# Kernel tuning notes

Hardware: AMD Instinct MI355X
Metric: run time of the kernel (lower is better)

Reference implementation:

```python
import jax, jax.numpy as jnp
import numpy as np

N = 50000      # num_nodes
R = 16         # num_relations
D = 200        # hidden_dim
E = 400000     # num_edges


def rgcn_layer(x, W, root, b, src, dst, etype):
    # Per-relation transform of all nodes: [R, N, D]
    xw = jnp.einsum('nd,rde->rne', x, W)
    # Per-edge message: gather transformed source feature for the edge's relation
    msg = xw[etype, src]                      # [E, D]
    # Mean aggregation per (relation, destination) pair, matching PyG RGCNConv aggr='mean'
    seg = etype * N + dst                     # composite segment id in [0, R*N)
    sums = jax.ops.segment_sum(msg, seg, num_segments=R * N)          # [R*N, D]
    cnt = jax.ops.segment_sum(jnp.ones((msg.shape[0],), x.dtype), seg,
                              num_segments=R * N)                     # [R*N]
    mean = sums / jnp.clip(cnt, 1.0)[:, None]
    agg = mean.reshape(R, N, -1).sum(0)       # sum over relations: [N, D]
    return agg + x @ root + b


def setup_inputs() -> dict:
    key = jax.random.key(0)
    ks = jax.random.split(key, 9)
    scale = 1.0 / np.sqrt(D)
    inp = {
        'edge_index': jax.random.randint(ks[0], (2, E), 0, N),
        'edge_type': jax.random.randint(ks[1], (E,), 0, R),
        'emb': jax.random.normal(ks[2], (N, D), jnp.float32),
        'W1': jax.random.normal(ks[3], (R, D, D), jnp.float32) * scale,
        'root1': jax.random.normal(ks[4], (D, D), jnp.float32) * scale,
        'b1': jnp.zeros((D,), jnp.float32),
        'W2': jax.random.normal(ks[5], (R, D, D), jnp.float32) * scale,
        'root2': jax.random.normal(ks[6], (D, D), jnp.float32) * scale,
        'b2': jnp.zeros((D,), jnp.float32),
    }
    return inp


def reference(edge_index, edge_type, emb, W1, root1, b1, W2, root2, b2):
    src, dst = edge_index[0], edge_index[1]
    h = rgcn_layer(emb, W1, root1, b1, src, dst, edge_type)
    h = jax.nn.relu(h)
    out = rgcn_layer(h, W2, root2, b2, src, dst, edge_type)
    return out
```

## Files before the change

### kernel.cpp

```cpp
#include <hip/hip_runtime.h>
#include <cstdint>
#include <cstddef>

#define NNODES 50000
#define NREL   16
#define DIM    200
#define NEDGE  400000
#define NBLK   782
#define NKEY   (NBLK * 1024)
#define NPART  (NKEY / 256)
#define WTREL  46592
#define WTSZ   (17 * WTREL)
#define MAXB   12
#define PCAP   1280
#define GTOT   119
#define BFRAG  13312

typedef __attribute__((ext_vector_type(8))) short short8;
typedef __attribute__((ext_vector_type(4))) float floatx4;

typedef __attribute__((address_space(1))) const unsigned int gas_u32;
typedef __attribute__((address_space(3))) unsigned int las_u32;

__device__ __forceinline__ unsigned short f2bf(float f) {
    unsigned int u = __float_as_uint(f);
    u = (u + 0x7FFFu + ((u >> 16) & 1u)) >> 16;
    return (unsigned short)u;
}
__device__ __forceinline__ float bf2f(unsigned short h) {
    return __uint_as_float(((unsigned int)h) << 16);
}


__device__ __forceinline__ int edge_key(int d, int r) {
    return (d >> 6) * 1024 + r * 64 + (d & 63);
}

__global__ void count_kernel(const int* __restrict__ ei, const int* __restrict__ et,
                             int* __restrict__ cnt) {
    int e = blockIdx.x * 256 + threadIdx.x;
    if (e < NEDGE) atomicAdd(&cnt[edge_key(ei[NEDGE + e], et[e])], 1);
}

__global__ void scan1_kernel(const int* __restrict__ cnt, int* __restrict__ rp,
                             int* __restrict__ part) {
    __shared__ int sc[256];
    int b = blockIdx.x, t = threadIdx.x, i = b * 256 + t;
    int v = cnt[i];
    sc[t] = v; __syncthreads();
    for (int off = 1; off < 256; off <<= 1) {
        int x = (t >= off) ? sc[t - off] : 0;
        __syncthreads();
        sc[t] += x;
        __syncthreads();
    }
    int incl = sc[t];
    rp[i] = incl - v;
    if (t == 255) part[b] = incl;
}

__global__ void scan2_kernel(int* __restrict__ p) {
    __shared__ int sc[256];
    __shared__ int carry_s;
    int t = threadIdx.x;
    if (t == 0) carry_s = 0;
    __syncthreads();
    for (int base = 0; base < NPART; base += 256) {
        int i = base + t;
        int v = (i < NPART) ? p[i] : 0;
        sc[t] = v; __syncthreads();
        for (int off = 1; off < 256; off <<= 1) {
            int x = (t >= off) ? sc[t - off] : 0;
            __syncthreads();
            sc[t] += x;
            __syncthreads();
        }
        int incl = sc[t];
        int carry = carry_s;
        if (i < NPART) p[i] = carry + incl - v;
        __syncthreads();
        if (t == 255) carry_s = carry + incl;
        __syncthreads();
    }
    if (t == 0) p[NPART] = carry_s;
}

__global__ void scan3_kernel(int* __restrict__ rp, int* __restrict__ cursor,
                             const int* __restrict__ part) {
    int i = blockIdx.x * 256 + threadIdx.x;
    if (i < NKEY) {
        int v = rp[i] + part[i >> 8];
        rp[i] = v;
        cursor[i] = v;
    } else if (i == NKEY) {
        rp[i] = part[NPART];
    }
}

__global__ void scatter_kernel(const int* __restrict__ ei, const int* __restrict__ et,
                               int* __restrict__ cursor, int* __restrict__ perm) {
    int e = blockIdx.x * 256 + threadIdx.x;
    if (e < NEDGE) {
        int d = ei[NEDGE + e];
        int pos = atomicAdd(&cursor[edge_key(d, et[e])], 1);
        perm[pos] = ((d & 63) << 16) | ei[e];
    }
}

__global__ void wt_kernel(const float* __restrict__ W, const float* __restrict__ root,
                          unsigned short* __restrict__ WT) {
    int idx = blockIdx.x * 256 + threadIdx.x;
    if (idx >= WTSZ) return;
    int r = idx / WTREL;
    int rem = idx - r * WTREL;
    int blk = rem >> 9;
    int within = rem & 511;
    int ks = blk / 13;
    int nt = blk - ks * 13;
    int lane = within >> 3;
    int j = within & 7;
    int mn = lane & 15, quad = lane >> 4;
    int n = nt * 16 + mn;
    int k = ks * 32 + quad * 8 + j;
    float v = 0.f;
    if (n < DIM && k < DIM)
        v = (r < 16) ? W[((size_t)r * DIM + k) * DIM + n] : root[(size_t)k * DIM + n];
    WT[idx] = f2bf(v);
}

template<bool SRC_F32, bool OUT_RELU_BF16>
__global__ __launch_bounds__(256, 2) void fused_kernel(
        const void* __restrict__ srcv, const unsigned short* __restrict__ WT,
        const int* __restrict__ rp, const int* __restrict__ perm,
        const float* __restrict__ bias, void* __restrict__ outv) {
    __shared__ __align__(16) char As[25664];
    __shared__ __align__(16) char Bs[2 * BFRAG];
    __shared__ int pLds[PCAP];
    const int t = threadIdx.x;
    const int w = t >> 6;
    const int lane = t & 63;
    const int quad = lane >> 4;
    const int mn = lane & 15;
    const int v0 = blockIdx.x * 64;
    const int kbase = blockIdx.x * 1024;
    const bool colok = (lane < 50);

    const int li = (lane < 16) ? lane : 15;
    const int b0 = rp[kbase + li * 64 + (w << 4)];
    const int b1 = rp[kbase + li * 64 + (w << 4) + 16];
    const int pbase = rp[kbase];
    const int pend  = rp[kbase + 1024];
    const int pcnt  = pend - pbase;
    const bool staged = (pcnt <= PCAP);

    for (int i = t; i < 25664 / 16; i += 256)
        *(float4*)(As + i * 16) = make_float4(0.f, 0.f, 0.f, 0.f);
    if (staged)
        for (int i = t; i < pcnt; i += 256) pLds[i] = perm[pbase + i];

    const float* srcf = (const float*)srcv;
    const unsigned short* srcb = (const unsigned short*)srcv;

    floatx4 acc[13];
    #pragma unroll
    for (int i = 0; i < 13; ++i) acc[i] = (floatx4){0.f, 0.f, 0.f, 0.f};

    auto stage_frag = [&](int g, int frag) {
        const char* src = (const char*)WT + ((size_t)(13 * g + frag) << 10) + (lane << 4);
        char* dst = Bs + (g & 1) * BFRAG + (frag << 10);
        __builtin_amdgcn_global_load_lds((gas_u32*)(const void*)src,
                                         (las_u32*)(void*)dst, 16, 0, 0);
    };
    auto stage = [&](int g) {
        #pragma unroll
        for (int i = 0; i < 3; ++i) stage_frag(g, (i << 2) + w);
        if (w == 0) stage_frag(g, 12);
    };
    auto process = [&](int g, int ks) {
        const short8 af = *(const short8*)(As + ((w << 4) + mn) * 400 + (quad << 4) + ks * 64);
        const char* bb = Bs + (g & 1) * BFRAG + (lane << 4);
        short8 bf[13];
        #pragma unroll
        for (int nt = 0; nt < 13; ++nt)
            bf[nt] = *(const short8*)(bb + nt * 1024);
        #pragma unroll
        for (int nt = 0; nt < 13; ++nt)
            acc[nt] = __builtin_amdgcn_mfma_f32_16x16x32_bf16(af, bf[nt], acc[nt], 0, 0, 0);
    };
    auto zero_rows = [&]() {
        char* base = As + w * 6400;
        #pragma unroll
        for (int i = 0; i < 6; ++i)
            *(float4*)(base + i * 1024 + lane * 16) = make_float4(0.f, 0.f, 0.f, 0.f);
        if (lane < 16)
            *(float4*)(base + 6144 + lane * 16) = make_float4(0.f, 0.f, 0.f, 0.f);
    };

    auto gather = [&](int rel) {
        zero_rows();
        if (rel < NREL) {
            const int ws = __builtin_amdgcn_readlane(b0, rel);
            const int we = __builtin_amdgcn_readlane(b1, rel);
            if (ws >= we) return;
            int curM = -1, curCnt = 0;
            float s0 = 0.f, s1 = 0.f, s2 = 0.f, s3 = 0.f;
            auto flush = [&]() {
                if (curM >= 0 && colok) {
                    float sc = 1.0f / (float)curCnt;
                    ushort4 pk;
                    pk.x = f2bf(s0 * sc); pk.y = f2bf(s1 * sc);
                    pk.z = f2bf(s2 * sc); pk.w = f2bf(s3 * sc);
                    *(ushort4*)(As + curM * 400 + lane * 8) = pk;
                }
            };
            for (int jb = ws; jb < we; jb += MAXB) {
                const int nb = min(we - jb, MAXB);
                const int sel = (lane < nb) ? lane : (nb - 1);
                int pmv;
                if (staged) pmv = pLds[jb - pbase + sel];
                else        pmv = perm[jb + sel];
                int pms[MAXB];
                #pragma unroll
                for (int i = 0; i < MAXB; ++i)
                    pms[i] = __builtin_amdgcn_readlane(pmv, i);
                float4  qf[MAXB];
                ushort4 qb[MAXB];
                #pragma unroll
                for (int i = 0; i < MAXB; ++i) {
                    if (i < nb && colok) {
                        const int sv = pms[i] & 0xFFFF;
                        if (SRC_F32) qf[i] = *(const float4*)(srcf + (size_t)sv * DIM + (lane << 2));
                        else         qb[i] = *(const ushort4*)(srcb + (size_t)sv * DIM + (lane << 2));
                    }
                }
                #pragma unroll
                for (int i = 0; i < MAXB; ++i) {
                    if (i < nb) {
                        const int m = pms[i] >> 16;
                        float f0, f1, f2, f3;
                        if (SRC_F32) { f0 = qf[i].x; f1 = qf[i].y; f2 = qf[i].z; f3 = qf[i].w; }
                        else { f0 = bf2f(qb[i].x); f1 = bf2f(qb[i].y); f2 = bf2f(qb[i].z); f3 = bf2f(qb[i].w); }
                        if (m != curM) {
                            flush();
                            curM = m; curCnt = 1;
                            s0 = f0; s1 = f1; s2 = f2; s3 = f3;
                        } else {
                            ++curCnt;
                            s0 += f0; s1 += f1; s2 += f2; s3 += f3;
                        }
                    }
                }
            }
            flush();
        } else {
            #pragma unroll
            for (int g2 = 0; g2 < 2; ++g2) {
                float4  qf[8];
                ushort4 qb[8];
                #pragma unroll
                for (int i = 0; i < 8; ++i) {
                    const int v = v0 + (w << 4) + g2 * 8 + i;
                    if (v < NNODES && colok) {
                        if (SRC_F32) qf[i] = *(const float4*)(srcf + (size_t)v * DIM + (lane << 2));
                        else         qb[i] = *(const ushort4*)(srcb + (size_t)v * DIM + (lane << 2));
                    }
                }
                #pragma unroll
                for (int i = 0; i < 8; ++i) {
                    const int m = (w << 4) + g2 * 8 + i;
                    if (v0 + m < NNODES && colok) {
                        ushort4 pk;
                        if (SRC_F32) {
                            pk.x = f2bf(qf[i].x); pk.y = f2bf(qf[i].y);
                            pk.z = f2bf(qf[i].z); pk.w = f2bf(qf[i].w);
                        } else pk = qb[i];
                        *(ushort4*)(As + m * 400 + lane * 8) = pk;
                    }
                }
            }
        }
    };

    stage(0);
    __syncthreads();

    int ks = 0, rel = 0;
    #pragma unroll 1
    for (int g = 0; g < GTOT; ++g) {
        if (g + 1 < GTOT) stage(g + 1);
        if (ks == 0) gather(rel);
        process(g, ks);
        __syncthreads();
        if (++ks == 7) { ks = 0; ++rel; }
    }

    float* outf = (float*)outv;
    unsigned short* outb = (unsigned short*)outv;
    #pragma unroll
    for (int nt = 0; nt < 13; ++nt) {
        const int col = nt * 16 + mn;
        if (col < DIM) {
            const float bv = bias[col];
            #pragma unroll
            for (int i = 0; i < 4; ++i) {
                const int v = v0 + (w << 4) + (quad << 2) + i;
                if (v < NNODES) {
                    float x = acc[nt][i] + bv;
                    if (OUT_RELU_BF16) {
                        x = fmaxf(x, 0.f);
                        outb[(size_t)v * DIM + col] = f2bf(x);
                    } else {
                        outf[(size_t)v * DIM + col] = x;
                    }
                }
            }
        }
    }
}


extern "C" void kernel_launch(void* const* d_in, const int* in_sizes, int n_in,
                              void* d_out, int out_size, void* d_ws, size_t ws_size,
                              hipStream_t stream) {
    const int*   edge_index = (const int*)d_in[0];
    const int*   edge_type  = (const int*)d_in[1];
    const float* emb   = (const float*)d_in[2];
    const float* W1    = (const float*)d_in[3];
    const float* root1 = (const float*)d_in[4];
    const float* b1    = (const float*)d_in[5];
    const float* W2    = (const float*)d_in[6];
    const float* root2 = (const float*)d_in[7];
    const float* b2    = (const float*)d_in[8];
    float* out = (float*)d_out;

    char* ws = (char*)d_ws;
    int*            cnt    = (int*)(ws);
    int*            cursor = (int*)(ws);
    int*            rp     = (int*)(ws + 3203072);
    int*            part   = (int*)(ws + 6406152);
    int*            perm   = (int*)(ws + 6418672);
    unsigned short* hbf    = (unsigned short*)(ws + 8018672);
    unsigned short* WT1    = (unsigned short*)(ws + 28018672);
    unsigned short* WT2    = (unsigned short*)(ws + 29602800);

    hipMemsetAsync(cnt, 0, (size_t)NKEY * sizeof(int), stream);
    count_kernel<<<(NEDGE + 255) / 256, 256, 0, stream>>>(edge_index, edge_type, cnt);
    scan1_kernel<<<NPART, 256, 0, stream>>>(cnt, rp, part);
    scan2_kernel<<<1, 256, 0, stream>>>(part);
    scan3_kernel<<<(NKEY + 256) / 256 + 1, 256, 0, stream>>>(rp, cursor, part);
    scatter_kernel<<<(NEDGE + 255) / 256, 256, 0, stream>>>(edge_index, edge_type, cursor, perm);

    wt_kernel<<<(WTSZ + 255) / 256, 256, 0, stream>>>(W1, root1, WT1);
    wt_kernel<<<(WTSZ + 255) / 256, 256, 0, stream>>>(W2, root2, WT2);

    fused_kernel<true, true><<<NBLK, 256, 0, stream>>>(emb, WT1, rp, perm, b1, hbf);
    fused_kernel<false, false><<<NBLK, 256, 0, stream>>>(hbf, WT2, rp, perm, b2, out);
}
```

Before: 633.8 us.

## Enlarge node tile to 224 rows per block with 7 waves and dual accumulators

```diff
diff --git a/kernel.cpp b/kernel.cpp
--- a/kernel.cpp
+++ b/kernel.cpp
@@ -6,15 +6,18 @@
 #define NREL   16
 #define DIM    200
 #define NEDGE  400000
-#define NBLK   782
-#define NKEY   (NBLK * 1024)
+#define BROWS  224
+#define NBLK   224
+#define KPB    3584
+#define NKEY   (NBLK * KPB)
 #define NPART  (NKEY / 256)
 #define WTREL  46592
 #define WTSZ   (17 * WTREL)
-#define MAXB   12
-#define PCAP   1280
+#define MAXB   16
+#define PCAP   2304
 #define GTOT   119
 #define BFRAG  13312
+#define ASZ    (BROWS * 400 + 64)
 
 typedef __attribute__((ext_vector_type(8))) short short8;
 typedef __attribute__((ext_vector_type(4))) float floatx4;
@@ -33,7 +36,7 @@
 
 
 __device__ __forceinline__ int edge_key(int d, int r) {
-    return (d >> 6) * 1024 + r * 64 + (d & 63);
+    return (d / BROWS) * KPB + r * BROWS + (d % BROWS);
 }
 
 __global__ void count_kernel(const int* __restrict__ ei, const int* __restrict__ et,
@@ -103,7 +106,7 @@
     if (e < NEDGE) {
         int d = ei[NEDGE + e];
         int pos = atomicAdd(&cursor[edge_key(d, et[e])], 1);
-        perm[pos] = ((d & 63) << 16) | ei[e];
+        perm[pos] = ((d % BROWS) << 16) | ei[e];
     }
 }
 
@@ -129,11 +132,11 @@
 }
 
 template<bool SRC_F32, bool OUT_RELU_BF16>
-__global__ __launch_bounds__(256, 2) void fused_kernel(
+__global__ __launch_bounds__(448, 2) void fused_kernel(
         const void* __restrict__ srcv, const unsigned short* __restrict__ WT,
         const int* __restrict__ rp, const int* __restrict__ perm,
         const float* __restrict__ bias, void* __restrict__ outv) {
-    __shared__ __align__(16) char As[25664];
+    __shared__ __align__(16) char As[ASZ];
     __shared__ __align__(16) char Bs[2 * BFRAG];
     __shared__ int pLds[PCAP];
     const int t = threadIdx.x;
@@ -141,29 +144,32 @@
     const int lane = t & 63;
     const int quad = lane >> 4;
     const int mn = lane & 15;
-    const int v0 = blockIdx.x * 64;
-    const int kbase = blockIdx.x * 1024;
+    const int v0 = blockIdx.x * BROWS;
+    const int kbase = blockIdx.x * KPB;
     const bool colok = (lane < 50);
 
     const int li = (lane < 16) ? lane : 15;
-    const int b0 = rp[kbase + li * 64 + (w << 4)];
-    const int b1 = rp[kbase + li * 64 + (w << 4) + 16];
+    const int b0 = rp[kbase + li * BROWS + (w << 5)];
+    const int b1 = rp[kbase + li * BROWS + (w << 5) + 32];
     const int pbase = rp[kbase];
-    const int pend  = rp[kbase + 1024];
+    const int pend  = rp[kbase + KPB];
     const int pcnt  = pend - pbase;
     const bool staged = (pcnt <= PCAP);
 
-    for (int i = t; i < 25664 / 16; i += 256)
+    for (int i = t; i < ASZ / 16; i += 448)
         *(float4*)(As + i * 16) = make_float4(0.f, 0.f, 0.f, 0.f);
     if (staged)
-        for (int i = t; i < pcnt; i += 256) pLds[i] = perm[pbase + i];
+        for (int i = t; i < pcnt; i += 448) pLds[i] = perm[pbase + i];
 
     const float* srcf = (const float*)srcv;
     const unsigned short* srcb = (const unsigned short*)srcv;
 
-    floatx4 acc[13];
+    floatx4 accA[13], accB[13];
     #pragma unroll
-    for (int i = 0; i < 13; ++i) acc[i] = (floatx4){0.f, 0.f, 0.f, 0.f};
+    for (int i = 0; i < 13; ++i) {
+        accA[i] = (floatx4){0.f, 0.f, 0.f, 0.f};
+        accB[i] = (floatx4){0.f, 0.f, 0.f, 0.f};
+    }
 
     auto stage_frag = [&](int g, int frag) {
         const char* src = (const char*)WT + ((size_t)(13 * g + frag) << 10) + (lane << 4);
@@ -172,28 +178,28 @@
                                          (las_u32*)(void*)dst, 16, 0, 0);
     };
     auto stage = [&](int g) {
+        stage_frag(g, w);
+        if (w < 6) stage_frag(g, w + 7);
+    };
+    auto process = [&](int g, int ks) {
+        const char* abase = As + ((w << 5) + mn) * 400 + (quad << 4) + ks * 64;
+        const short8 af0 = *(const short8*)(abase);
+        const short8 af1 = *(const short8*)(abase + 16 * 400);
+        const char* bb = Bs + (g & 1) * BFRAG + (lane << 4);
         #pragma unroll
-        for (int i = 0; i < 3; ++i) stage_frag(g, (i << 2) + w);
-        if (w == 0) stage_frag(g, 12);
-    };
-    auto process = [&](int g, int ks) {
-        const short8 af = *(const short8*)(As + ((w << 4) + mn) * 400 + (quad << 4) + ks * 64);
-        const char* bb = Bs + (g & 1) * BFRAG + (lane << 4);
-        short8 bf[13];
+        for (int nt = 0; nt < 13; ++nt) {
+            const short8 bf = *(const short8*)(bb + nt * 1024);
+            accA[nt] = __builtin_amdgcn_mfma_f32_16x16x32_bf16(af0, bf, accA[nt], 0, 0, 0);
+            accB[nt] = __builtin_amdgcn_mfma_f32_16x16x32_bf16(af1, bf, accB[nt], 0, 0, 0);
+        }
+    };
+    auto zero_rows = [&]() {
+        char* base = As + w * 12800;
         #pragma unroll
-        for (int nt = 0; nt < 13; ++nt)
-            bf[nt] = *(const short8*)(bb + nt * 1024);
-        #pragma unroll
-        for (int nt = 0; nt < 13; ++nt)
-            acc[nt] = __builtin_amdgcn_mfma_f32_16x16x32_bf16(af, bf[nt], acc[nt], 0, 0, 0);
-    };
-    auto zero_rows = [&]() {
-        char* base = As + w * 6400;
-        #pragma unroll
-        for (int i = 0; i < 6; ++i)
+        for (int i = 0; i < 12; ++i)
             *(float4*)(base + i * 1024 + lane * 16) = make_float4(0.f, 0.f, 0.f, 0.f);
-        if (lane < 16)
-            *(float4*)(base + 6144 + lane * 16) = make_float4(0.f, 0.f, 0.f, 0.f);
+        if (lane < 32)
+            *(float4*)(base + 12288 + lane * 16) = make_float4(0.f, 0.f, 0.f, 0.f);
     };
 
     auto gather = [&](int rel) {
@@ -254,12 +260,12 @@
             flush();
         } else {
             #pragma unroll
-            for (int g2 = 0; g2 < 2; ++g2) {
+            for (int g2 = 0; g2 < 4; ++g2) {
                 float4  qf[8];
                 ushort4 qb[8];
                 #pragma unroll
                 for (int i = 0; i < 8; ++i) {
-                    const int v = v0 + (w << 4) + g2 * 8 + i;
+                    const int v = v0 + (w << 5) + g2 * 8 + i;
                     if (v < NNODES && colok) {
                         if (SRC_F32) qf[i] = *(const float4*)(srcf + (size_t)v * DIM + (lane << 2));
                         else         qb[i] = *(const ushort4*)(srcb + (size_t)v * DIM + (lane << 2));
@@ -267,7 +273,7 @@
                 }
                 #pragma unroll
                 for (int i = 0; i < 8; ++i) {
-                    const int m = (w << 4) + g2 * 8 + i;
+                    const int m = (w << 5) + g2 * 8 + i;
                     if (v0 + m < NNODES && colok) {
                         ushort4 pk;
                         if (SRC_F32) {
@@ -303,14 +309,25 @@
             const float bv = bias[col];
             #pragma unroll
             for (int i = 0; i < 4; ++i) {
-                const int v = v0 + (w << 4) + (quad << 2) + i;
-                if (v < NNODES) {
-                    float x = acc[nt][i] + bv;
+                const int m  = (w << 5) + (quad << 2) + i;
+                const int vA = v0 + m;
+                const int vB = vA + 16;
+                if (vA < NNODES) {
+                    float x = accA[nt][i] + bv;
                     if (OUT_RELU_BF16) {
                         x = fmaxf(x, 0.f);
-                        outb[(size_t)v * DIM + col] = f2bf(x);
+                        outb[(size_t)vA * DIM + col] = f2bf(x);
                     } else {
-                        outf[(size_t)v * DIM + col] = x;
+                        outf[(size_t)vA * DIM + col] = x;
+                    }
+                }
+                if (vB < NNODES) {
+                    float x = accB[nt][i] + bv;
+                    if (OUT_RELU_BF16) {
+                        x = fmaxf(x, 0.f);
+                        outb[(size_t)vB * DIM + col] = f2bf(x);
+                    } else {
+                        outf[(size_t)vB * DIM + col] = x;
                     }
                 }
             }
@@ -334,14 +351,14 @@
     float* out = (float*)d_out;
 
     char* ws = (char*)d_ws;
-    int*            cnt    = (int*)(ws);
-    int*            cursor = (int*)(ws);
-    int*            rp     = (int*)(ws + 3203072);
-    int*            part   = (int*)(ws + 6406152);
-    int*            perm   = (int*)(ws + 6418672);
-    unsigned short* hbf    = (unsigned short*)(ws + 8018672);
-    unsigned short* WT1    = (unsigned short*)(ws + 28018672);
-    unsigned short* WT2    = (unsigned short*)(ws + 29602800);
+    unsigned short* WT1    = (unsigned short*)(ws);
+    unsigned short* WT2    = (unsigned short*)(ws + 1584128);
+    int*            rp     = (int*)(ws + 3168256);
+    int*            perm   = (int*)(ws + 6379536);
+    unsigned short* hbf    = (unsigned short*)(ws + 7979536);
+    int*            cnt    = (int*)(ws + 7979536);
+    int*            cursor = (int*)(ws + 7979536);
+    int*            part   = (int*)(ws + 7979536 + 3211264);
 
     hipMemsetAsync(cnt, 0, (size_t)NKEY * sizeof(int), stream);
     count_kernel<<<(NEDGE + 255) / 256, 256, 0, stream>>>(edge_index, edge_type, cnt);
@@ -353,6 +370,6 @@
     wt_kernel<<<(WTSZ + 255) / 256, 256, 0, stream>>>(W1, root1, WT1);
     wt_kernel<<<(WTSZ + 255) / 256, 256, 0, stream>>>(W2, root2, WT2);
 
-    fused_kernel<true, true><<<NBLK, 256, 0, stream>>>(emb, WT1, rp, perm, b1, hbf);
-    fused_kernel<false, false><<<NBLK, 256, 0, stream>>>(hbf, WT2, rp, perm, b2, out);
-}
+    fused_kernel<true, true><<<NBLK, 448, 0, stream>>>(emb, WT1, rp, perm, b1, hbf);
+    fused_kernel<false, false><<<NBLK, 448, 0, stream>>>(hbf, WT2, rp, perm, b2, out);
+}
```

Result: faster. 560.4 us (-11.6%).
